# Performance work log

Measured on AMD Instinct MI355X. Metric: run time of the kernel, lower is better.

Reference implementation:

```python
import jax, jax.numpy as jnp
import numpy as np

ALPHA = 1.0
BETA = 1.0
GAMMA = 1.0
EPS = 1e-08

D = 128      # feature / hash-code dim
N = 4096     # number of items


def setup_inputs() -> dict:
    key = jax.random.key(0)
    k = jax.random.split(key, 6)
    return {
        "SU": jax.random.uniform(k[0], (N, N, 1), dtype=jnp.float32),
        "SP": jax.random.uniform(k[1], (N, N, 1), dtype=jnp.float32),
        "SM": jax.random.uniform(k[2], (N, N, 1), dtype=jnp.float32),
        "FP": jax.random.uniform(k[3], (D, N), dtype=jnp.float32),
        "FM": jax.random.uniform(k[4], (D, N), dtype=jnp.float32),
        "B": jax.random.uniform(k[5], (D, N), dtype=jnp.float32),
    }


def reference(SU, SP, SM, FP, FM, B):
    # IRSC: Omega_U = FP^T FM / 2, sum over all (i,j) of -S*Omega + log(1+Omega)
    omega_u = jnp.einsum('di,dj->ij', FP, FM) * 0.5          # [N, N]
    loss_irsc = jnp.sum(-SU[:, :, 0] * omega_u + jnp.log1p(omega_u))

    # IASC: same form on FP^T FP and FM^T FM, with epsilon inside the log
    omega_p = jnp.einsum('di,dj->ij', FP, FP) * 0.5
    omega_m = jnp.einsum('di,dj->ij', FM, FM) * 0.5
    loss_sp = jnp.sum(-SP[:, :, 0] * omega_p + jnp.log(1.0 + omega_p + EPS))
    loss_sm = jnp.sum(-SM[:, :, 0] * omega_m + jnp.log(1.0 + omega_m + EPS))
    loss_iasc = loss_sp + loss_sm

    # BQC: Frobenius norms (not squared)
    loss_bqc = jnp.sqrt(jnp.sum((FP - B) ** 2)) + jnp.sqrt(jnp.sum((FM - B) ** 2))

    # FDC: ||F @ ones||_F^2 = sum over rows of (row-sum)^2
    loss_fdc = jnp.sum(jnp.sum(FP, axis=1) ** 2) + jnp.sum(jnp.sum(FM, axis=1) ** 2)

    return loss_irsc + ALPHA * loss_iasc + BETA * loss_bqc + GAMMA * loss_fdc
```

## Files before the change

kernel.cpp:

```cpp
#include <hip/hip_runtime.h>
#include <hip/hip_bf16.h>
#include <math.h>

#define NN 4096
#define DD 128

typedef __attribute__((ext_vector_type(8))) short bf16x8;
typedef __attribute__((ext_vector_type(4))) float f32x4;


__device__ __forceinline__ void gload_lds16(const float* g, float* l) {
    __builtin_amdgcn_global_load_lds((const __attribute__((address_space(1))) char*)g,
                                     (__attribute__((address_space(3))) char*)l, 16, 0, 0);
}

__global__ __launch_bounds__(256)
void convert_t_kernel(const float* __restrict__ FP, const float* __restrict__ FM,
                      __hip_bfloat16* __restrict__ FPt, __hip_bfloat16* __restrict__ FMt)
{
    const float* src = blockIdx.y ? FM : FP;
    __hip_bfloat16* dst = blockIdx.y ? FMt : FPt;
    const int t  = threadIdx.x;
    const int il = t & 127;
    const int dh = t >> 7;
    const int i  = blockIdx.x * 128 + il;
    #pragma unroll
    for (int it = 0; it < 8; ++it) {
        const int d0 = dh * 64 + it * 8;
        union { __hip_bfloat162 h[4]; bf16x8 v; } p;
        #pragma unroll
        for (int j = 0; j < 4; ++j) {
            const float a = src[(long)(d0 + 2*j)     * NN + i];
            const float b = src[(long)(d0 + 2*j + 1) * NN + i];
            p.h[j] = __float22bfloat162_rn(make_float2(a, b));
        }
        *(bf16x8*)&dst[(long)i * DD + d0] = p.v;
    }
}

__global__ __launch_bounds__(256, 2)
void gemm_loss_fused(const float* __restrict__ SU, const float* __restrict__ SP,
                     const float* __restrict__ SM,
                     const __hip_bfloat16* __restrict__ FPt_,
                     const __hip_bfloat16* __restrict__ FMt_,
                     double* __restrict__ accum)
{
    __shared__ float sS[4][2][32 * 32];
    const int t0   = threadIdx.x;
    const int lane = t0 & 63, wid = t0 >> 6;
    const int l15  = lane & 15, l4 = lane >> 4;
    const int w    = blockIdx.x * 4 + wid;
    const int jt   = w & 127, rr = w >> 7;
    const int j0   = jt * 32;
    const short* FPt = (const short*)FPt_;
    const short* FMt = (const short*)FMt_;

    bf16x8 bgP[2][4], bgM[2][4];
    #pragma unroll
    for (int n = 0; n < 2; ++n)
        #pragma unroll
        for (int kb = 0; kb < 4; ++kb) {
            const long off = (long)(j0 + n * 16 + l15) * DD + kb * 32 + l4 * 8;
            bgP[n][kb] = *(const bf16x8*)&FPt[off];
            bgM[n][kb] = *(const bf16x8*)&FMt[off];
        }

    float lsum = 0.f;
    bf16x8 afA[2][4], afB[2][4];

#define TILE_Z(tt)   ((tt) >> 3)
#define TILE_I0(tt)  ((rr + (((tt) & 7) << 4)) << 5)

#define ISSUE_AF(tt, dstbuf)                                                   \
    {                                                                          \
        const int z_  = TILE_Z(tt);                                            \
        const int i0_ = TILE_I0(tt);                                           \
        const short* Fa_ = (z_ == 2) ? FMt : FPt;                              \
        _Pragma("unroll")                                                      \
        for (int m = 0; m < 2; ++m)                                            \
            _Pragma("unroll")                                                  \
            for (int kb = 0; kb < 4; ++kb)                                     \
                dstbuf[m][kb] = *(const bf16x8*)&Fa_[(long)(i0_ + m * 16 + l15) * DD + kb * 32 + l4 * 8]; \
    }

#define ISSUE_STAGE(tt)                                                        \
    {                                                                          \
        const int z_  = TILE_Z(tt);                                            \
        const int i0_ = TILE_I0(tt);                                           \
        const float* S_ = (z_ == 0) ? SU : (z_ == 1) ? SP : SM;                \
        const float* src_ = S_ + (long)(i0_ + (lane >> 3)) * NN + j0 + (lane & 7) * 4; \
        float* dst_ = &sS[wid][(tt) & 1][0];                                   \
        _Pragma("unroll")                                                      \
        for (int q_ = 0; q_ < 4; ++q_)                                         \
            gload_lds16(src_ + (long)q_ * 8 * NN, dst_ + q_ * 256);            \
    }

#define TILE_BODY(tt, cur, nxt)                                                \
    {                                                                          \
        const int tc = (tt);                                                   \
        const int tn = (tc < 23) ? tc + 1 : 23;                                \
        ISSUE_AF(tn, nxt);                                                     \
        __builtin_amdgcn_sched_barrier(0);                                     \
        ISSUE_STAGE(tn);                                                       \
        __builtin_amdgcn_sched_barrier(0);                                     \
        asm volatile("s_waitcnt vmcnt(12)");                                   \
        __builtin_amdgcn_sched_barrier(0);                                     \
        const int z_  = TILE_Z(tc);                                            \
        f32x4 acc[2][2] = {};                                                  \
        if (z_ == 1) {                                                         \
            _Pragma("unroll")                                                  \
            for (int kb = 0; kb < 4; ++kb)                                     \
                _Pragma("unroll")                                              \
                for (int m = 0; m < 2; ++m)                                    \
                    _Pragma("unroll")                                          \
                    for (int n = 0; n < 2; ++n)                                \
                        acc[m][n] = __builtin_amdgcn_mfma_f32_16x16x32_bf16(cur[m][kb], bgP[n][kb], acc[m][n], 0, 0, 0); \
        } else {                                                               \
            _Pragma("unroll")                                                  \
            for (int kb = 0; kb < 4; ++kb)                                     \
                _Pragma("unroll")                                              \
                for (int m = 0; m < 2; ++m)                                    \
                    _Pragma("unroll")                                          \
                    for (int n = 0; n < 2; ++n)                                \
                        acc[m][n] = __builtin_amdgcn_mfma_f32_16x16x32_bf16(cur[m][kb], bgM[n][kb], acc[m][n], 0, 0, 0); \
        }                                                                      \
        const float onep = (z_ == 0) ? 1.0f : 1.0f + 1e-8f;                    \
        const float* q = &sS[wid][tc & 1][0];                                  \
        _Pragma("unroll")                                                      \
        for (int m = 0; m < 2; ++m)                                            \
            _Pragma("unroll")                                                  \
            for (int n = 0; n < 2; ++n)                                        \
                _Pragma("unroll")                                              \
                for (int r = 0; r < 4; ++r) {                                  \
                    const float s = q[(m * 16 + l4 * 4 + r) * 32 + n * 16 + l15]; \
                    const float o = 0.5f * acc[m][n][r];                       \
                    lsum += fmaf(-s, o, __logf(o + onep));                     \
                }                                                              \
    }

    ISSUE_AF(0, afA);
    ISSUE_STAGE(0);

    #pragma unroll 1
    for (int t = 0; t < 24; t += 2) {
        TILE_BODY(t,     afA, afB);
        TILE_BODY(t + 1, afB, afA);
    }
#undef TILE_BODY
#undef ISSUE_STAGE
#undef ISSUE_AF
#undef TILE_Z
#undef TILE_I0

    float v = lsum;
    #pragma unroll
    for (int off = 32; off; off >>= 1) v += __shfl_down(v, off);
    if (lane == 0)
        atomicAdd(accum + ((w & 15) << 3), (double)v);
}

__global__ __launch_bounds__(256, 2)
void gemm_loss_mfma(const float* __restrict__ S, const float* __restrict__ F1,
                    const float* __restrict__ F2, float eps, double* __restrict__ accum)
{
    __shared__ char lds[2][128 * 256];
    __shared__ float red[4];
    const int t  = threadIdx.x;
    const int i0 = blockIdx.y * 128;
    const int j0 = blockIdx.x * 128;
    {
        const int il   = t & 127;
        const int half = t >> 7;
        const float* c1 = F1 + i0 + il;
        const float* c2 = F2 + j0 + il;
        char* r1 = lds[0] + il * 256;
        char* r2 = lds[1] + il * 256;
        #pragma unroll
        for (int it = 0; it < 8; ++it) {
            const int q  = half * 8 + it;
            const int d0 = q * 8;
            float a[8], b[8];
            #pragma unroll
            for (int j = 0; j < 8; ++j) {
                a[j] = c1[(long)(d0 + j) * NN];
                b[j] = c2[(long)(d0 + j) * NN];
            }
            union { __hip_bfloat162 h[4]; bf16x8 v; } pa, pb;
            #pragma unroll
            for (int j = 0; j < 4; ++j) {
                pa.h[j] = __float22bfloat162_rn(make_float2(a[2*j], a[2*j+1]));
                pb.h[j] = __float22bfloat162_rn(make_float2(b[2*j], b[2*j+1]));
            }
            const int off = (q ^ (il & 15)) << 4;
            *(bf16x8*)(r1 + off) = pa.v;
            *(bf16x8*)(r2 + off) = pb.v;
        }
    }
    __syncthreads();
    const int lane = t & 63;
    const int wid  = t >> 6;
    const int wr   = wid >> 1, wc = wid & 1;
    const int l15  = lane & 15, l4 = lane >> 4;
    float sreg[4][4][4];
    #pragma unroll
    for (int am = 0; am < 4; ++am)
        #pragma unroll
        for (int r = 0; r < 4; ++r) {
            const long gi    = (long)(i0 + wr * 64 + am * 16 + l4 * 4 + r);
            const long basep = gi * NN + j0 + wc * 64 + l15;
            #pragma unroll
            for (int bn = 0; bn < 4; ++bn)
                sreg[am][bn][r] = S[basep + bn * 16];
        }
    f32x4 acc[4][4] = {};
    #pragma unroll
    for (int kb = 0; kb < 4; ++kb) {
        bf16x8 af[4], bgr[4];
        #pragma unroll
        for (int m = 0; m < 4; ++m) {
            const int ia = wr * 64 + m * 16 + l15;
            af[m] = *(const bf16x8*)(lds[0] + ia * 256 + (((kb * 4 + l4) ^ l15) << 4));
            const int jbq = wc * 64 + m * 16 + l15;
            bgr[m] = *(const bf16x8*)(lds[1] + jbq * 256 + (((kb * 4 + l4) ^ l15) << 4));
        }
        #pragma unroll
        for (int m = 0; m < 4; ++m)
            #pragma unroll
            for (int n = 0; n < 4; ++n)
                acc[m][n] = __builtin_amdgcn_mfma_f32_16x16x32_bf16(af[m], bgr[n], acc[m][n], 0, 0, 0);
    }
    float lsum = 0.f;
    #pragma unroll
    for (int m = 0; m < 4; ++m)
        #pragma unroll
        for (int n = 0; n < 4; ++n)
            #pragma unroll
            for (int r = 0; r < 4; ++r) {
                const float o = 0.5f * acc[m][n][r];
                lsum += fmaf(-sreg[m][n][r], o, __logf(1.0f + o + eps));
            }
    float v = lsum;
    #pragma unroll
    for (int off = 32; off; off >>= 1) v += __shfl_down(v, off);
    if ((t & 63) == 0) red[t >> 6] = v;
    __syncthreads();
    if (t == 0) {
        const float tot = red[0] + red[1] + red[2] + red[3];
        atomicAdd(accum, (double)tot);
    }
}

__global__ __launch_bounds__(256)
void bqc_kernel(const float* __restrict__ FP, const float* __restrict__ FM,
                const float* __restrict__ B, double* __restrict__ ws)
{
    __shared__ float red1[4], red2[4];
    const int n4 = DD * NN / 4;
    float s1 = 0.f, s2 = 0.f;
    for (int i = blockIdx.x * blockDim.x + threadIdx.x; i < n4;
         i += gridDim.x * blockDim.x) {
        const float4 p = ((const float4*)FP)[i];
        const float4 m = ((const float4*)FM)[i];
        const float4 b = ((const float4*)B)[i];
        float d;
        d = p.x - b.x; s1 += d * d;  d = p.y - b.y; s1 += d * d;
        d = p.z - b.z; s1 += d * d;  d = p.w - b.w; s1 += d * d;
        d = m.x - b.x; s2 += d * d;  d = m.y - b.y; s2 += d * d;
        d = m.z - b.z; s2 += d * d;  d = m.w - b.w; s2 += d * d;
    }
    const int t = threadIdx.x;
    #pragma unroll
    for (int off = 32; off; off >>= 1) {
        s1 += __shfl_down(s1, off);
        s2 += __shfl_down(s2, off);
    }
    if ((t & 63) == 0) { red1[t >> 6] = s1; red2[t >> 6] = s2; }
    __syncthreads();
    if (t == 0) {
        atomicAdd(&ws[128], (double)(red1[0] + red1[1] + red1[2] + red1[3]));
        atomicAdd(&ws[129], (double)(red2[0] + red2[1] + red2[2] + red2[3]));
    }
}

__global__ __launch_bounds__(256)
void fdc_kernel(const float* __restrict__ FP, const float* __restrict__ FM,
                double* __restrict__ ws)
{
    __shared__ float red[4];
    const float* F = (blockIdx.x >= DD) ? FM : FP;
    const int row = blockIdx.x & (DD - 1);
    float s = 0.f;
    const float4* rowp = (const float4*)&F[(long)row * NN];
    for (int i = threadIdx.x; i < NN / 4; i += blockDim.x) {
        const float4 v = rowp[i];
        s += v.x + v.y + v.z + v.w;
    }
    const int t = threadIdx.x;
    #pragma unroll
    for (int off = 32; off; off >>= 1) s += __shfl_down(s, off);
    if ((t & 63) == 0) red[t >> 6] = s;
    __syncthreads();
    if (t == 0) {
        const double rs = (double)(red[0] + red[1] + red[2] + red[3]);
        atomicAdd(&ws[130], rs * rs);
    }
}

__global__ void finalize_kernel(const double* __restrict__ ws, float* __restrict__ out)
{
    if (threadIdx.x == 0 && blockIdx.x == 0) {
        double s = 0.0;
        #pragma unroll
        for (int k = 0; k < 16; ++k) s += ws[k * 8];
        out[0] = (float)(s + ws[130] + sqrt(ws[128]) + sqrt(ws[129]));
    }
}

extern "C" void kernel_launch(void* const* d_in, const int* in_sizes, int n_in,
                              void* d_out, int out_size, void* d_ws, size_t ws_size,
                              hipStream_t stream)
{
    const float* SU = (const float*)d_in[0];
    const float* SP = (const float*)d_in[1];
    const float* SM = (const float*)d_in[2];
    const float* FP = (const float*)d_in[3];
    const float* FM = (const float*)d_in[4];
    const float* B  = (const float*)d_in[5];
    float*  out = (float*)d_out;
    double* ws  = (double*)d_ws;

    hipMemsetAsync(d_ws, 0, 4096, stream);

    const size_t fb   = (size_t)NN * DD * sizeof(__hip_bfloat16);
    const size_t need = 4096 + 2 * fb;

    if (ws_size >= need) {
        char* base = (char*)d_ws + 4096;
        __hip_bfloat16* FPt = (__hip_bfloat16*)(base);
        __hip_bfloat16* FMt = (__hip_bfloat16*)(base + fb);
        convert_t_kernel<<<dim3(NN / 128, 2), 256, 0, stream>>>(FP, FM, FPt, FMt);
        gemm_loss_fused<<<512, 256, 0, stream>>>(SU, SP, SM, FPt, FMt, ws);
    } else {
        dim3 grid(NN / 128, NN / 128);
        gemm_loss_mfma<<<grid, 256, 0, stream>>>(SU, FP, FM, 0.0f, ws);
        gemm_loss_mfma<<<grid, 256, 0, stream>>>(SP, FP, FP, 1e-8f, ws);
        gemm_loss_mfma<<<grid, 256, 0, stream>>>(SM, FM, FM, 1e-8f, ws);
    }
    bqc_kernel<<<512, 256, 0, stream>>>(FP, FM, B, ws);
    fdc_kernel<<<256, 256, 0, stream>>>(FP, FM, ws);
    finalize_kernel<<<1, 64, 0, stream>>>(ws, out);
}
```

Baseline: 92.58 us.

## Deepen S staging to four buffers, batch LDS reads, fuse BQC into convert

```diff
diff --git a/kernel.cpp b/kernel.cpp
--- a/kernel.cpp
+++ b/kernel.cpp
@@ -7,35 +7,52 @@
 
 typedef __attribute__((ext_vector_type(8))) short bf16x8;
 typedef __attribute__((ext_vector_type(4))) float f32x4;
+#define AS3 __attribute__((address_space(3)))
 
 
 __device__ __forceinline__ void gload_lds16(const float* g, float* l) {
     __builtin_amdgcn_global_load_lds((const __attribute__((address_space(1))) char*)g,
-                                     (__attribute__((address_space(3))) char*)l, 16, 0, 0);
+                                     (AS3 char*)l, 16, 0, 0);
 }
 
 __global__ __launch_bounds__(256)
-void convert_t_kernel(const float* __restrict__ FP, const float* __restrict__ FM,
-                      __hip_bfloat16* __restrict__ FPt, __hip_bfloat16* __restrict__ FMt)
-{
-    const float* src = blockIdx.y ? FM : FP;
-    __hip_bfloat16* dst = blockIdx.y ? FMt : FPt;
+void convert_bqc_kernel(const float* __restrict__ FP, const float* __restrict__ FM,
+                        const float* __restrict__ B,
+                        __hip_bfloat16* __restrict__ FPt, __hip_bfloat16* __restrict__ FMt,
+                        double* __restrict__ ws)
+{
+    const int y = blockIdx.y;
+    const float* src = y ? FM : FP;
+    __hip_bfloat16* dst = y ? FMt : FPt;
     const int t  = threadIdx.x;
     const int il = t & 127;
     const int dh = t >> 7;
     const int i  = blockIdx.x * 128 + il;
+    float s = 0.f;
     #pragma unroll
     for (int it = 0; it < 8; ++it) {
         const int d0 = dh * 64 + it * 8;
+        float a[8];
+        #pragma unroll
+        for (int j = 0; j < 8; ++j) {
+            a[j] = src[(long)(d0 + j) * NN + i];
+            const float b = B[(long)(d0 + j) * NN + i];
+            const float d = a[j] - b;
+            s += d * d;
+        }
         union { __hip_bfloat162 h[4]; bf16x8 v; } p;
         #pragma unroll
-        for (int j = 0; j < 4; ++j) {
-            const float a = src[(long)(d0 + 2*j)     * NN + i];
-            const float b = src[(long)(d0 + 2*j + 1) * NN + i];
-            p.h[j] = __float22bfloat162_rn(make_float2(a, b));
-        }
+        for (int j = 0; j < 4; ++j)
+            p.h[j] = __float22bfloat162_rn(make_float2(a[2*j], a[2*j+1]));
         *(bf16x8*)&dst[(long)i * DD + d0] = p.v;
     }
+    __shared__ float red[4];
+    #pragma unroll
+    for (int off = 32; off; off >>= 1) s += __shfl_down(s, off);
+    if ((t & 63) == 0) red[t >> 6] = s;
+    __syncthreads();
+    if (t == 0)
+        atomicAdd(&ws[128 + y], (double)(red[0] + red[1] + red[2] + red[3]));
 }
 
 __global__ __launch_bounds__(256, 2)
@@ -45,7 +62,7 @@
                      const __hip_bfloat16* __restrict__ FMt_,
                      double* __restrict__ accum)
 {
-    __shared__ float sS[4][2][32 * 32];
+    __shared__ float sS[4][4][1024];
     const int t0   = threadIdx.x;
     const int lane = t0 & 63, wid = t0 >> 6;
     const int l15  = lane & 15, l4 = lane >> 4;
@@ -64,6 +81,9 @@
             bgP[n][kb] = *(const bf16x8*)&FPt[off];
             bgM[n][kb] = *(const bf16x8*)&FMt[off];
         }
+
+    const unsigned sbase =
+        (unsigned)(unsigned long long)(AS3 float*)&sS[wid][0][l4 * 128 + l15];
 
     float lsum = 0.f;
     bf16x8 afA[2][4], afB[2][4];
@@ -83,29 +103,31 @@
                 dstbuf[m][kb] = *(const bf16x8*)&Fa_[(long)(i0_ + m * 16 + l15) * DD + kb * 32 + l4 * 8]; \
     }
 
-#define ISSUE_STAGE(tt)                                                        \
+#define ISSUE_STAGE(srcT, dbuf)                                                \
     {                                                                          \
-        const int z_  = TILE_Z(tt);                                            \
-        const int i0_ = TILE_I0(tt);                                           \
+        const int z_  = TILE_Z(srcT);                                          \
+        const int i0_ = TILE_I0(srcT);                                         \
         const float* S_ = (z_ == 0) ? SU : (z_ == 1) ? SP : SM;                \
         const float* src_ = S_ + (long)(i0_ + (lane >> 3)) * NN + j0 + (lane & 7) * 4; \
-        float* dst_ = &sS[wid][(tt) & 1][0];                                   \
+        float* d_ = &sS[wid][dbuf][0];                                         \
         _Pragma("unroll")                                                      \
         for (int q_ = 0; q_ < 4; ++q_)                                         \
-            gload_lds16(src_ + (long)q_ * 8 * NN, dst_ + q_ * 256);            \
-    }
+            gload_lds16(src_ + (long)q_ * 8 * NN, d_ + q_ * 256);              \
+    }
+
+#define DSR(dst, OFF) asm volatile("ds_read_b32 %0, %1 offset:" #OFF \
+                                   : "=v"(dst) : "v"(lpb))
 
 #define TILE_BODY(tt, cur, nxt)                                                \
     {                                                                          \
         const int tc = (tt);                                                   \
-        const int tn = (tc < 23) ? tc + 1 : 23;                                \
-        ISSUE_AF(tn, nxt);                                                     \
-        __builtin_amdgcn_sched_barrier(0);                                     \
-        ISSUE_STAGE(tn);                                                       \
-        __builtin_amdgcn_sched_barrier(0);                                     \
-        asm volatile("s_waitcnt vmcnt(12)");                                   \
-        __builtin_amdgcn_sched_barrier(0);                                     \
-        const int z_  = TILE_Z(tc);                                            \
+        ISSUE_AF((tc < 23) ? tc + 1 : 23, nxt);                                \
+        __builtin_amdgcn_sched_barrier(0);                                     \
+        ISSUE_STAGE((tc + 3 < 24) ? tc + 3 : 23, (tc + 3) & 3);                \
+        __builtin_amdgcn_sched_barrier(0);                                     \
+        asm volatile("s_waitcnt vmcnt(16)");                                   \
+        __builtin_amdgcn_sched_barrier(0);                                     \
+        const int z_ = TILE_Z(tc);                                             \
         f32x4 acc[2][2] = {};                                                  \
         if (z_ == 1) {                                                         \
             _Pragma("unroll")                                                  \
@@ -124,22 +146,35 @@
                     for (int n = 0; n < 2; ++n)                                \
                         acc[m][n] = __builtin_amdgcn_mfma_f32_16x16x32_bf16(cur[m][kb], bgM[n][kb], acc[m][n], 0, 0, 0); \
         }                                                                      \
+        __builtin_amdgcn_sched_barrier(0);                                     \
+        const unsigned lpb = sbase + (unsigned)((tc & 3) * 4096);              \
+        float sv[2][2][4];                                                     \
+        DSR(sv[0][0][0], 0);    DSR(sv[0][0][1], 128);                         \
+        DSR(sv[0][0][2], 256);  DSR(sv[0][0][3], 384);                         \
+        DSR(sv[0][1][0], 64);   DSR(sv[0][1][1], 192);                         \
+        DSR(sv[0][1][2], 320);  DSR(sv[0][1][3], 448);                         \
+        DSR(sv[1][0][0], 2048); DSR(sv[1][0][1], 2176);                        \
+        DSR(sv[1][0][2], 2304); DSR(sv[1][0][3], 2432);                        \
+        DSR(sv[1][1][0], 2112); DSR(sv[1][1][1], 2240);                        \
+        DSR(sv[1][1][2], 2368); DSR(sv[1][1][3], 2496);                        \
+        asm volatile("s_waitcnt lgkmcnt(0)");                                  \
+        __builtin_amdgcn_sched_barrier(0);                                     \
         const float onep = (z_ == 0) ? 1.0f : 1.0f + 1e-8f;                    \
-        const float* q = &sS[wid][tc & 1][0];                                  \
         _Pragma("unroll")                                                      \
         for (int m = 0; m < 2; ++m)                                            \
             _Pragma("unroll")                                                  \
             for (int n = 0; n < 2; ++n)                                        \
                 _Pragma("unroll")                                              \
                 for (int r = 0; r < 4; ++r) {                                  \
-                    const float s = q[(m * 16 + l4 * 4 + r) * 32 + n * 16 + l15]; \
                     const float o = 0.5f * acc[m][n][r];                       \
-                    lsum += fmaf(-s, o, __logf(o + onep));                     \
+                    lsum += fmaf(-sv[m][n][r], o, __logf(o + onep));           \
                 }                                                              \
     }
 
+    ISSUE_STAGE(0, 0);
+    ISSUE_STAGE(1, 1);
     ISSUE_AF(0, afA);
-    ISSUE_STAGE(0);
+    ISSUE_STAGE(2, 2);
 
     #pragma unroll 1
     for (int t = 0; t < 24; t += 2) {
@@ -147,6 +182,7 @@
         TILE_BODY(t + 1, afB, afA);
     }
 #undef TILE_BODY
+#undef DSR
 #undef ISSUE_STAGE
 #undef ISSUE_AF
 #undef TILE_Z
@@ -338,15 +374,16 @@
         char* base = (char*)d_ws + 4096;
         __hip_bfloat16* FPt = (__hip_bfloat16*)(base);
         __hip_bfloat16* FMt = (__hip_bfloat16*)(base + fb);
-        convert_t_kernel<<<dim3(NN / 128, 2), 256, 0, stream>>>(FP, FM, FPt, FMt);
+        convert_bqc_kernel<<<dim3(NN / 128, 2), 256, 0, stream>>>(FP, FM, B, FPt, FMt, ws);
         gemm_loss_fused<<<512, 256, 0, stream>>>(SU, SP, SM, FPt, FMt, ws);
+        fdc_kernel<<<256, 256, 0, stream>>>(FP, FM, ws);
     } else {
         dim3 grid(NN / 128, NN / 128);
         gemm_loss_mfma<<<grid, 256, 0, stream>>>(SU, FP, FM, 0.0f, ws);
         gemm_loss_mfma<<<grid, 256, 0, stream>>>(SP, FP, FP, 1e-8f, ws);
         gemm_loss_mfma<<<grid, 256, 0, stream>>>(SM, FM, FM, 1e-8f, ws);
-    }
-    bqc_kernel<<<512, 256, 0, stream>>>(FP, FM, B, ws);
-    fdc_kernel<<<256, 256, 0, stream>>>(FP, FM, ws);
+        bqc_kernel<<<512, 256, 0, stream>>>(FP, FM, B, ws);
+        fdc_kernel<<<256, 256, 0, stream>>>(FP, FM, ws);
+    }
     finalize_kernel<<<1, 64, 0, stream>>>(ws, out);
 }
```

Measured after the change: 97.37 us. +5.2%, slower.

## Split fused GEMM-loss into bf16 Omega materialization plus streaming consume kernel

Applied to the files above, without the earlier changes.

```diff
diff --git a/kernel.cpp b/kernel.cpp
--- a/kernel.cpp
+++ b/kernel.cpp
@@ -7,35 +7,133 @@
 
 typedef __attribute__((ext_vector_type(8))) short bf16x8;
 typedef __attribute__((ext_vector_type(4))) float f32x4;
+#define AS3 __attribute__((address_space(3)))
 
 
 __device__ __forceinline__ void gload_lds16(const float* g, float* l) {
     __builtin_amdgcn_global_load_lds((const __attribute__((address_space(1))) char*)g,
-                                     (__attribute__((address_space(3))) char*)l, 16, 0, 0);
+                                     (AS3 char*)l, 16, 0, 0);
 }
 
 __global__ __launch_bounds__(256)
-void convert_t_kernel(const float* __restrict__ FP, const float* __restrict__ FM,
-                      __hip_bfloat16* __restrict__ FPt, __hip_bfloat16* __restrict__ FMt)
-{
-    const float* src = blockIdx.y ? FM : FP;
-    __hip_bfloat16* dst = blockIdx.y ? FMt : FPt;
+void convert_bqc_kernel(const float* __restrict__ FP, const float* __restrict__ FM,
+                        const float* __restrict__ B,
+                        __hip_bfloat16* __restrict__ FPt, __hip_bfloat16* __restrict__ FMt,
+                        double* __restrict__ ws)
+{
+    const int y = blockIdx.y;
+    const float* src = y ? FM : FP;
+    __hip_bfloat16* dst = y ? FMt : FPt;
     const int t  = threadIdx.x;
     const int il = t & 127;
     const int dh = t >> 7;
     const int i  = blockIdx.x * 128 + il;
+    float s = 0.f;
     #pragma unroll
     for (int it = 0; it < 8; ++it) {
         const int d0 = dh * 64 + it * 8;
+        float a[8];
+        #pragma unroll
+        for (int j = 0; j < 8; ++j) {
+            a[j] = src[(long)(d0 + j) * NN + i];
+            const float b = B[(long)(d0 + j) * NN + i];
+            const float d = a[j] - b;
+            s += d * d;
+        }
         union { __hip_bfloat162 h[4]; bf16x8 v; } p;
         #pragma unroll
-        for (int j = 0; j < 4; ++j) {
-            const float a = src[(long)(d0 + 2*j)     * NN + i];
-            const float b = src[(long)(d0 + 2*j + 1) * NN + i];
-            p.h[j] = __float22bfloat162_rn(make_float2(a, b));
-        }
+        for (int j = 0; j < 4; ++j)
+            p.h[j] = __float22bfloat162_rn(make_float2(a[2*j], a[2*j+1]));
         *(bf16x8*)&dst[(long)i * DD + d0] = p.v;
     }
+    __shared__ float red[4];
+    #pragma unroll
+    for (int off = 32; off; off >>= 1) s += __shfl_down(s, off);
+    if ((t & 63) == 0) red[t >> 6] = s;
+    __syncthreads();
+    if (t == 0)
+        atomicAdd(&ws[128 + y], (double)(red[0] + red[1] + red[2] + red[3]));
+}
+
+__global__ __launch_bounds__(256, 2)
+void omega_kernel(const __hip_bfloat16* __restrict__ FPt_,
+                  const __hip_bfloat16* __restrict__ FMt_,
+                  __hip_bfloat16* __restrict__ Om_)
+{
+    const int t = threadIdx.x;
+    const int lane = t & 63, wid = t >> 6;
+    const int wr = wid >> 1, wc = wid & 1;
+    const int l15 = lane & 15, l4 = lane >> 4;
+    const int z  = blockIdx.z;
+    const int i0 = blockIdx.y * 128 + wr * 64;
+    const int j0 = blockIdx.x * 128 + wc * 64;
+    const short* Fi = (const short*)((z == 2) ? FMt_ : FPt_);
+    const short* Fj = (const short*)((z == 0) ? FMt_ : (z == 1) ? FPt_ : FMt_);
+    unsigned short* Om = (unsigned short*)Om_ + (long)z * NN * NN;
+
+    bf16x8 ai[4][4], bj[4][4];
+    #pragma unroll
+    for (int m = 0; m < 4; ++m)
+        #pragma unroll
+        for (int kb = 0; kb < 4; ++kb) {
+            ai[m][kb] = *(const bf16x8*)&Fi[(long)(i0 + m * 16 + l15) * DD + kb * 32 + l4 * 8];
+            bj[m][kb] = *(const bf16x8*)&Fj[(long)(j0 + m * 16 + l15) * DD + kb * 32 + l4 * 8];
+        }
+    f32x4 acc[4][4] = {};
+    #pragma unroll
+    for (int kb = 0; kb < 4; ++kb)
+        #pragma unroll
+        for (int m = 0; m < 4; ++m)
+            #pragma unroll
+            for (int n = 0; n < 4; ++n)
+                acc[m][n] = __builtin_amdgcn_mfma_f32_16x16x32_bf16(bj[n][kb], ai[m][kb], acc[m][n], 0, 0, 0);
+    #pragma unroll
+    for (int m = 0; m < 4; ++m)
+        #pragma unroll
+        for (int n = 0; n < 4; ++n) {
+            union { __hip_bfloat162 h[2]; uint2 u; } p;
+            p.h[0] = __float22bfloat162_rn(make_float2(0.5f * acc[m][n][0], 0.5f * acc[m][n][1]));
+            p.h[1] = __float22bfloat162_rn(make_float2(0.5f * acc[m][n][2], 0.5f * acc[m][n][3]));
+            *(uint2*)&Om[(long)(i0 + m * 16 + l15) * NN + j0 + n * 16 + l4 * 4] = p.u;
+        }
+}
+
+__global__ __launch_bounds__(256)
+void consume_kernel(const float* __restrict__ SU, const float* __restrict__ SP,
+                    const float* __restrict__ SM,
+                    const __hip_bfloat16* __restrict__ Om_,
+                    double* __restrict__ accum)
+{
+    const unsigned* Om = (const unsigned*)Om_;
+    const long seg = (long)NN * NN / 8;
+    float lsum = 0.f;
+    const long step = (long)gridDim.x * 256;
+    for (long e = blockIdx.x * 256 + threadIdx.x; e < 3 * seg; e += step) {
+        const int z = (int)(e >> 21);
+        const long off = e & (seg - 1);
+        const float* Sp = ((z == 0) ? SU : (z == 1) ? SP : SM) + off * 8;
+        const float onep = (z == 0) ? 1.0f : 1.0f + 1e-8f;
+        const float4 s0 = *(const float4*)Sp;
+        const float4 s1 = *(const float4*)(Sp + 4);
+        const uint4 q = *(const uint4*)&Om[(long)z * ((long)NN * NN / 2) + off * 4];
+#define TERM(w, slo, shi)                                                      \
+        {                                                                      \
+            const float o0 = __uint_as_float((w) << 16);                       \
+            const float o1 = __uint_as_float((w) & 0xFFFF0000u);               \
+            lsum += fmaf(-(slo), o0, __logf(o0 + onep));                       \
+            lsum += fmaf(-(shi), o1, __logf(o1 + onep));                       \
+        }
+        TERM(q.x, s0.x, s0.y)
+        TERM(q.y, s0.z, s0.w)
+        TERM(q.z, s1.x, s1.y)
+        TERM(q.w, s1.z, s1.w)
+#undef TERM
+    }
+    float v = lsum;
+    #pragma unroll
+    for (int off = 32; off; off >>= 1) v += __shfl_down(v, off);
+    if ((threadIdx.x & 63) == 0)
+        atomicAdd(accum + ((blockIdx.x & 15) << 3), (double)v);
 }
 
 __global__ __launch_bounds__(256, 2)
@@ -70,7 +168,6 @@
 
 #define TILE_Z(tt)   ((tt) >> 3)
 #define TILE_I0(tt)  ((rr + (((tt) & 7) << 4)) << 5)
-
 #define ISSUE_AF(tt, dstbuf)                                                   \
     {                                                                          \
         const int z_  = TILE_Z(tt);                                            \
@@ -82,7 +179,6 @@
             for (int kb = 0; kb < 4; ++kb)                                     \
                 dstbuf[m][kb] = *(const bf16x8*)&Fa_[(long)(i0_ + m * 16 + l15) * DD + kb * 32 + l4 * 8]; \
     }
-
 #define ISSUE_STAGE(tt)                                                        \
     {                                                                          \
         const int z_  = TILE_Z(tt);                                            \
@@ -94,7 +190,6 @@
         for (int q_ = 0; q_ < 4; ++q_)                                         \
             gload_lds16(src_ + (long)q_ * 8 * NN, dst_ + q_ * 256);            \
     }
-
 #define TILE_BODY(tt, cur, nxt)                                                \
     {                                                                          \
         const int tc = (tt);                                                   \
@@ -140,7 +235,6 @@
 
     ISSUE_AF(0, afA);
     ISSUE_STAGE(0);
-
     #pragma unroll 1
     for (int t = 0; t < 24; t += 2) {
         TILE_BODY(t,     afA, afB);
@@ -215,11 +309,11 @@
     f32x4 acc[4][4] = {};
     #pragma unroll
     for (int kb = 0; kb < 4; ++kb) {
-        bf16x8 af[4], bgr[4];
+        bf16x8 afl[4], bgr[4];
         #pragma unroll
         for (int m = 0; m < 4; ++m) {
             const int ia = wr * 64 + m * 16 + l15;
-            af[m] = *(const bf16x8*)(lds[0] + ia * 256 + (((kb * 4 + l4) ^ l15) << 4));
+            afl[m] = *(const bf16x8*)(lds[0] + ia * 256 + (((kb * 4 + l4) ^ l15) << 4));
             const int jbq = wc * 64 + m * 16 + l15;
             bgr[m] = *(const bf16x8*)(lds[1] + jbq * 256 + (((kb * 4 + l4) ^ l15) << 4));
         }
@@ -227,7 +321,7 @@
         for (int m = 0; m < 4; ++m)
             #pragma unroll
             for (int n = 0; n < 4; ++n)
-                acc[m][n] = __builtin_amdgcn_mfma_f32_16x16x32_bf16(af[m], bgr[n], acc[m][n], 0, 0, 0);
+                acc[m][n] = __builtin_amdgcn_mfma_f32_16x16x32_bf16(afl[m], bgr[n], acc[m][n], 0, 0, 0);
     }
     float lsum = 0.f;
     #pragma unroll
@@ -331,22 +425,31 @@
 
     hipMemsetAsync(d_ws, 0, 4096, stream);
 
-    const size_t fb   = (size_t)NN * DD * sizeof(__hip_bfloat16);
-    const size_t need = 4096 + 2 * fb;
-
-    if (ws_size >= need) {
+    const size_t fb       = (size_t)NN * DD * sizeof(__hip_bfloat16);
+    const size_t om_bytes = (size_t)3 * NN * NN * sizeof(__hip_bfloat16);
+    const size_t need_sm  = 4096 + 2 * fb;
+    const size_t need_big = need_sm + om_bytes;
+
+    if (ws_size >= need_sm) {
         char* base = (char*)d_ws + 4096;
         __hip_bfloat16* FPt = (__hip_bfloat16*)(base);
         __hip_bfloat16* FMt = (__hip_bfloat16*)(base + fb);
-        convert_t_kernel<<<dim3(NN / 128, 2), 256, 0, stream>>>(FP, FM, FPt, FMt);
-        gemm_loss_fused<<<512, 256, 0, stream>>>(SU, SP, SM, FPt, FMt, ws);
+        convert_bqc_kernel<<<dim3(NN / 128, 2), 256, 0, stream>>>(FP, FM, B, FPt, FMt, ws);
+        if (ws_size >= need_big) {
+            __hip_bfloat16* Om = (__hip_bfloat16*)(base + 2 * fb);
+            omega_kernel<<<dim3(NN / 128, NN / 128, 3), 256, 0, stream>>>(FPt, FMt, Om);
+            consume_kernel<<<2048, 256, 0, stream>>>(SU, SP, SM, Om, ws);
+        } else {
+            gemm_loss_fused<<<512, 256, 0, stream>>>(SU, SP, SM, FPt, FMt, ws);
+        }
+        fdc_kernel<<<256, 256, 0, stream>>>(FP, FM, ws);
     } else {
         dim3 grid(NN / 128, NN / 128);
         gemm_loss_mfma<<<grid, 256, 0, stream>>>(SU, FP, FM, 0.0f, ws);
         gemm_loss_mfma<<<grid, 256, 0, stream>>>(SP, FP, FP, 1e-8f, ws);
         gemm_loss_mfma<<<grid, 256, 0, stream>>>(SM, FM, FM, 1e-8f, ws);
-    }
-    bqc_kernel<<<512, 256, 0, stream>>>(FP, FM, B, ws);
-    fdc_kernel<<<256, 256, 0, stream>>>(FP, FM, ws);
+        bqc_kernel<<<512, 256, 0, stream>>>(FP, FM, B, ws);
+        fdc_kernel<<<256, 256, 0, stream>>>(FP, FM, ws);
+    }
     finalize_kernel<<<1, 64, 0, stream>>>(ws, out);
 }
```

Result: slower. 159.9 us (+72.8%).
